# Kernel optimization log

Hardware: AMD Instinct MI355X
Metric: run time of the kernel (lower is better)

Reference implementation:

```python
import jax, jax.numpy as jnp
import numpy as np

B, S, D, H = 2, 4096, 1024, 16
DH = D // H            # head dim = 64
W = 256                # one-sided attention window (attention_window // 2)
NC = S // W            # number of query chunks
NEG = -1e9


def setup_inputs() -> dict:
    key = jax.random.key(0)
    ks = jax.random.split(key, 8)
    sc = 0.02
    return {
        "hidden_states": jax.random.normal(ks[0], (B, S, D), jnp.float32),
        # additive float mask: 0 = local token, <0 = padding, >0 = global. All zeros here.
        "attention_mask": jnp.zeros((B, 1, 1, S), jnp.float32),
        "Wq": jax.random.normal(ks[1], (D, D), jnp.float32) * sc,
        "bq": jnp.zeros((D,), jnp.float32),
        "Wk": jax.random.normal(ks[2], (D, D), jnp.float32) * sc,
        "bk": jnp.zeros((D,), jnp.float32),
        "Wv": jax.random.normal(ks[3], (D, D), jnp.float32) * sc,
        "bv": jnp.zeros((D,), jnp.float32),
        "Wo": jax.random.normal(ks[4], (D, D), jnp.float32) * sc,
        "bo": jnp.zeros((D,), jnp.float32),
    }


def _heads(x, w, b):
    # [B,S,D] -> [B,H,S,DH]
    return (x @ w + b).reshape(B, S, H, DH).transpose(0, 2, 1, 3)


def _forward(hidden_states, attention_mask, Wq, bq, Wk, bk, Wv, bv, Wo, bo):
    mask = attention_mask[:, 0, 0, :]                    # [B,S] additive key mask
    q = _heads(hidden_states, Wq, bq) / jnp.sqrt(jnp.float32(DH))
    k = _heads(hidden_states, Wk, bk)
    v = _heads(hidden_states, Wv, bv)

    # Overlapping key/value chunks: chunk c covers padded positions [c*W, c*W+3W),
    # i.e. global keys [c*W - W, c*W + 2W) -- the union of the windows of its W queries.
    idx = jnp.arange(NC)[:, None] * W + jnp.arange(3 * W)[None, :]   # [NC,3W] into padded axis
    k_pad = jnp.pad(k, ((0, 0), (0, 0), (W, W), (0, 0)))
    v_pad = jnp.pad(v, ((0, 0), (0, 0), (W, W), (0, 0)))
    k_ch = k_pad[:, :, idx]                               # [B,H,NC,3W,DH]
    v_ch = v_pad[:, :, idx]                               # [B,H,NC,3W,DH]
    mask_ch = jnp.pad(mask, ((0, 0), (W, W)))[:, idx]     # [B,NC,3W]

    q_ch = q.reshape(B, H, NC, W, DH)
    scores = jnp.einsum('bhcqd,bhckd->bhcqk', q_ch, k_ch)  # [B,H,NC,W,3W]

    # Band mask: query local p attends key local o with 0 <= o - p <= 2W.
    rel = jnp.arange(3 * W)[None, :] - jnp.arange(W)[:, None]        # [W,3W]
    band = (rel >= 0) & (rel <= 2 * W)
    key_gidx = idx - W                                               # global key index
    valid = (key_gidx >= 0) & (key_gidx < S)                         # [NC,3W]
    allowed = band[None, :, :] & valid[:, None, :]                   # [NC,W,3W]

    scores = scores + mask_ch[:, None, :, None, :]
    scores = jnp.where(allowed[None, None], scores, NEG)
    probs = jax.nn.softmax(scores, axis=-1)

    out = jnp.einsum('bhcqk,bhckd->bhcqd', probs, v_ch)    # [B,H,NC,W,DH]
    out = out.reshape(B, H, S, DH).transpose(0, 2, 1, 3).reshape(B, S, D)
    return out @ Wo + bo


def reference(hidden_states, attention_mask, Wq, bq, Wk, bk, Wv, bv, Wo, bo):
    return _forward(hidden_states, attention_mask, Wq, bq, Wk, bk, Wv, bv, Wo, bo)
```

## Files before the change

kernel.cpp:

```cpp
#include <hip/hip_runtime.h>

typedef unsigned short u16;
typedef __bf16 bf16x8 __attribute__((ext_vector_type(8)));
typedef u16 u16x8 __attribute__((ext_vector_type(8)));
typedef float f32x4 __attribute__((ext_vector_type(4)));

#define LOG2E 1.4426950408889634f

static __device__ __forceinline__ u16 f2bf(float f) {
    union { float f; unsigned u; } x; x.f = f;
    unsigned r = x.u + 0x7fffu + ((x.u >> 16) & 1u);
    return (u16)(r >> 16);
}

static __device__ __forceinline__ void gl_lds16(const void* g, void* l) {
    __builtin_amdgcn_global_load_lds(
        (const __attribute__((address_space(1))) void*)g,
        (__attribute__((address_space(3))) void*)l, 16, 0, 0);
}

__global__ __launch_bounds__(256) void cvt_k(const float* __restrict__ src,
                                             u16* __restrict__ dst, int n) {
    int i = (blockIdx.x * 256 + threadIdx.x) * 4;
    if (i < n) {
        float4 v = *(const float4*)(src + i);
        ushort4 o;
        o.x = f2bf(v.x); o.y = f2bf(v.y); o.z = f2bf(v.z); o.w = f2bf(v.w);
        *(ushort4*)(dst + i) = o;
    }
}

__global__ __launch_bounds__(256) void transw_k(const float* __restrict__ w0,
                                                const float* __restrict__ w1,
                                                const float* __restrict__ w2,
                                                const float* __restrict__ w3,
                                                u16* __restrict__ wt) {
    __shared__ float T[64][65];
    const float* src = (blockIdx.z == 0) ? w0 : (blockIdx.z == 1) ? w1
                     : (blockIdx.z == 2) ? w2 : w3;
    u16* dst = wt + (size_t)blockIdx.z * 1048576;
    const int k0 = blockIdx.x * 64, n0 = blockIdx.y * 64;
    const int rr = threadIdx.x >> 6, col = threadIdx.x & 63;
#pragma unroll
    for (int i = 0; i < 16; ++i) {
        int row = i * 4 + rr;
        T[row][col] = src[(size_t)(k0 + row) * 1024 + n0 + col];
    }
    __syncthreads();
#pragma unroll
    for (int i = 0; i < 16; ++i) {
        int row = i * 4 + rr;
        dst[(size_t)(n0 + row) * 1024 + k0 + col] = f2bf(T[col][row]);
    }
}

__global__ __launch_bounds__(256, 2) void gemm_k(
    const u16* __restrict__ A, const u16* __restrict__ WT0,
    const float* __restrict__ b0, const float* __restrict__ b1,
    const float* __restrict__ b2,
    u16* __restrict__ o0, u16* __restrict__ o1, u16* __restrict__ o2,
    float* __restrict__ oF, int mode) {
    __shared__ alignas(16) u16 Al[128 * 32];
    __shared__ alignas(16) u16 Bl[128 * 32];

    const int tid = threadIdx.x;
    const int lane = tid & 63;
    const int wv = tid >> 6;
    const int wr = wv >> 1, wc = wv & 1;
    const int l15 = lane & 15, l4 = lane >> 4;

    const int mbase = blockIdx.x * 128;
    const int sel = blockIdx.y >> 3;
    const int nb = (blockIdx.y & 7) * 128;

    const u16* Ab = A + (size_t)mbase * 1024;
    const u16* Bb = WT0 + (size_t)sel * 1048576 + (size_t)nb * 1024;

    const int srow = tid >> 2;
    const int scol = (tid & 3) * 8;

    f32x4 acc[4][4] = {};

    for (int k0 = 0; k0 < 1024; k0 += 32) {
        char* la = (char*)Al + wv * 1024;
        char* lb = (char*)Bl + wv * 1024;
        gl_lds16(Ab + (size_t)srow * 1024 + k0 + scol, la);
        gl_lds16(Ab + (size_t)(srow + 64) * 1024 + k0 + scol, la + 4096);
        gl_lds16(Bb + (size_t)srow * 1024 + k0 + scol, lb);
        gl_lds16(Bb + (size_t)(srow + 64) * 1024 + k0 + scol, lb + 4096);
        __syncthreads();

        bf16x8 af[4], bfr[4];
#pragma unroll
        for (int mr = 0; mr < 4; ++mr)
            af[mr] = *(const bf16x8*)(Al + (wr * 64 + mr * 16 + l15) * 32 + l4 * 8);
#pragma unroll
        for (int nr = 0; nr < 4; ++nr)
            bfr[nr] = *(const bf16x8*)(Bl + (wc * 64 + nr * 16 + l15) * 32 + l4 * 8);
#pragma unroll
        for (int mr = 0; mr < 4; ++mr)
#pragma unroll
            for (int nr = 0; nr < 4; ++nr)
                acc[mr][nr] = __builtin_amdgcn_mfma_f32_16x16x32_bf16(
                    af[mr], bfr[nr], acc[mr][nr], 0, 0, 0);
        __syncthreads();
    }

    const float* bias = (sel == 0) ? b0 : ((sel == 1) ? b1 : b2);
    u16* oH = (sel == 0) ? o0 : ((sel == 1) ? o1 : o2);
    const float scale = (mode == 0 && sel == 0) ? 0.125f * LOG2E : 1.0f;

#pragma unroll
    for (int mr = 0; mr < 4; ++mr)
#pragma unroll
        for (int nr = 0; nr < 4; ++nr) {
            int col = nb + wc * 64 + nr * 16 + l15;
            float bv_ = bias[col];
#pragma unroll
            for (int j = 0; j < 4; ++j) {
                int row = mbase + wr * 64 + mr * 16 + l4 * 4 + j;
                float v = (acc[mr][nr][j] + bv_) * scale;
                if (mode == 0) {
                    int b_ = row >> 12, s_ = row & 4095;
                    int h_ = col >> 6, d_ = col & 63;
                    oH[(((size_t)(b_ * 16 + h_) * 4096) + s_) * 64 + d_] = f2bf(v);
                } else {
                    oF[(size_t)row * 1024 + col] = v;
                }
            }
        }
}

__global__ __launch_bounds__(512, 2) void attn_k(
    const u16* __restrict__ Qh, const u16* __restrict__ Kh,
    const u16* __restrict__ Vh, const float* __restrict__ mask,
    u16* __restrict__ attnb) {
    __shared__ alignas(16) u16 Kt[2][4096];
    __shared__ alignas(16) u16 Vt[2][4096];
    __shared__ alignas(16) u16 Pl[8][16][72];
    __shared__ float maskl[2][64];

    const int tid = threadIdx.x;
    const int lane = tid & 63;
    const int wv = tid >> 6;
    const int blk = blockIdx.x;
    const int c = blk & 15;
    const int h = (blk >> 4) & 15;
    const int b = blk >> 8;

    const size_t bh = (size_t)(b * 16 + h) * 4096;
    const u16* Qb = Qh + bh * 64;
    const u16* Kb = Kh + bh * 64;
    const u16* Vb = Vh + bh * 64;

    const int l15 = lane & 15;
    const int l4 = lane >> 4;
    const int qbase = c * 256 + wv * 32;

    bf16x8 qf[2][2];
#pragma unroll
    for (int mr = 0; mr < 2; ++mr) {
        int qs = qbase + mr * 16 + l15;
#pragma unroll
        for (int kk = 0; kk < 2; ++kk)
            qf[mr][kk] = *(const bf16x8*)(Qb + (size_t)qs * 64 + kk * 32 + l4 * 8);
    }

    f32x4 Ov[2][4] = {};
    float lpart[2][4] = {};
    float m = -3.0e38f;

    const int kkey = tid >> 3;
    const int kpos = tid & 7;
    const int vd0 = (tid & 7) * 8;
    const int vbx = (kkey >> 3) ^ (tid & 7);

    const int tmin = wv >> 1;
    const int tmax_t = (wv * 32 + 543) >> 6;

    {
        const int gk0 = c * 256 - 256;
        int gkk = min(max(gk0 + kkey, 0), 4095);
        gl_lds16(Kb + (size_t)gkk * 64 + ((kpos ^ (kkey & 7)) * 8), &Kt[0][wv * 512]);
        u16x8 vv = *(const u16x8*)(Vb + (size_t)gkk * 64 + vd0);
#pragma unroll
        for (int e = 0; e < 8; ++e)
            Vt[0][(vd0 + e) * 64 + ((vbx ^ e) * 8) + (kkey & 7)] = vv[e];
        if (tid < 64) {
            int gm = gk0 + tid;
            maskl[0][tid] = (gm >= 0 && gm < 4096) ? mask[b * 4096 + gm] * LOG2E : -3.0e9f;
        }
    }
    __syncthreads();

    for (int t = 0; t < 12; ++t) {
        const int cur = t & 1, nxt = cur ^ 1;
        const int gk0 = c * 256 - 256 + t * 64;
        const bool pre = (t + 1 < 12);

        u16x8 vv = {};
        float mval = 0.f;
        if (pre) {
            const int gk0n = gk0 + 64;
            int gkk = min(max(gk0n + kkey, 0), 4095);
            gl_lds16(Kb + (size_t)gkk * 64 + ((kpos ^ (kkey & 7)) * 8), &Kt[nxt][wv * 512]);
            vv = *(const u16x8*)(Vb + (size_t)gkk * 64 + vd0);
            if (tid < 64) {
                int gm = gk0n + tid;
                mval = (gm >= 0 && gm < 4096) ? mask[b * 4096 + gm] * LOG2E : -3.0e9f;
            }
        }

        if (t >= tmin && t <= tmax_t) {
            f32x4 sc[2][4] = {};
#pragma unroll
            for (int kk = 0; kk < 2; ++kk)
#pragma unroll
                for (int nr = 0; nr < 4; ++nr) {
                    int r = nr * 16 + l15;
                    bf16x8 kf = *(const bf16x8*)(&Kt[cur][r * 64 + (((kk * 4 + l4) ^ (r & 7)) * 8)]);
                    sc[0][nr] = __builtin_amdgcn_mfma_f32_16x16x32_bf16(qf[0][kk], kf, sc[0][nr], 0, 0, 0);
                    sc[1][nr] = __builtin_amdgcn_mfma_f32_16x16x32_bf16(qf[1][kk], kf, sc[1][nr], 0, 0, 0);
                }

            float amv[4]; int relb[4];
#pragma unroll
            for (int nr = 0; nr < 4; ++nr) {
                amv[nr] = maskl[cur][nr * 16 + l15];
                relb[nr] = gk0 + nr * 16 + l15 - qbase + 256;
            }

            float tmx = -3.0e9f;
#pragma unroll
            for (int mr = 0; mr < 2; ++mr)
#pragma unroll
                for (int nr = 0; nr < 4; ++nr)
#pragma unroll
                    for (int j = 0; j < 4; ++j) {
                        float sv = sc[mr][nr][j] + amv[nr];
                        unsigned u = (unsigned)(relb[nr] - (mr * 16 + l4 * 4 + j));
                        sv = (u <= 512u) ? sv : -3.0e9f;
                        sc[mr][nr][j] = sv;
                        tmx = fmaxf(tmx, sv);
                    }
            tmx = fmaxf(tmx, __shfl_xor(tmx, 1));
            tmx = fmaxf(tmx, __shfl_xor(tmx, 2));
            tmx = fmaxf(tmx, __shfl_xor(tmx, 4));
            tmx = fmaxf(tmx, __shfl_xor(tmx, 8));
            tmx = fmaxf(tmx, __shfl_xor(tmx, 16));
            tmx = fmaxf(tmx, __shfl_xor(tmx, 32));

            if (tmx > m) {
                float alpha = exp2f(m - tmx);
                m = tmx;
#pragma unroll
                for (int mr = 0; mr < 2; ++mr) {
#pragma unroll
                    for (int nd = 0; nd < 4; ++nd) Ov[mr][nd] *= alpha;
#pragma unroll
                    for (int j = 0; j < 4; ++j) lpart[mr][j] *= alpha;
                }
            }

#pragma unroll
            for (int mr = 0; mr < 2; ++mr)
#pragma unroll
                for (int j = 0; j < 4; ++j) {
                    float s0 = 0.f;
#pragma unroll
                    for (int nr = 0; nr < 4; ++nr) {
                        float p = exp2f(sc[mr][nr][j] - m);
                        sc[mr][nr][j] = p;
                        s0 += p;
                    }
                    lpart[mr][j] += s0;
                }

#pragma unroll
            for (int mr = 0; mr < 2; ++mr) {
#pragma unroll
                for (int nr = 0; nr < 4; ++nr)
#pragma unroll
                    for (int j = 0; j < 4; ++j)
                        Pl[wv][l4 * 4 + j][nr * 16 + l15] = f2bf(sc[mr][nr][j]);
#pragma unroll
                for (int kk = 0; kk < 2; ++kk) {
                    bf16x8 pf = *(const bf16x8*)(&Pl[wv][l15][kk * 32 + l4 * 8]);
#pragma unroll
                    for (int nd = 0; nd < 4; ++nd) {
                        int r2 = nd * 16 + l15;
                        bf16x8 vf = *(const bf16x8*)(&Vt[cur][r2 * 64 +
                            (((kk * 4 + l4) ^ (r2 & 7) ^ ((r2 >> 3) & 7)) * 8)]);
                        Ov[mr][nd] = __builtin_amdgcn_mfma_f32_16x16x32_bf16(pf, vf, Ov[mr][nd], 0, 0, 0);
                    }
                }
            }
        }

        if (pre) {
#pragma unroll
            for (int e = 0; e < 8; ++e)
                Vt[nxt][(vd0 + e) * 64 + ((vbx ^ e) * 8) + (kkey & 7)] = vv[e];
            if (tid < 64) maskl[nxt][tid] = mval;
        }
        __syncthreads();
    }

#pragma unroll
    for (int mr = 0; mr < 2; ++mr)
#pragma unroll
        for (int j = 0; j < 4; ++j) {
            float lr = lpart[mr][j];
            lr += __shfl_xor(lr, 1);
            lr += __shfl_xor(lr, 2);
            lr += __shfl_xor(lr, 4);
            lr += __shfl_xor(lr, 8);
            float inv = 1.0f / lr;
            int qs = qbase + mr * 16 + l4 * 4 + j;
            size_t rowb = ((size_t)b * 4096 + qs) * 1024;
#pragma unroll
            for (int nd = 0; nd < 4; ++nd)
                attnb[rowb + h * 64 + nd * 16 + l15] = f2bf(Ov[mr][nd][j] * inv);
        }
}

extern "C" void kernel_launch(void* const* d_in, const int* in_sizes, int n_in,
                              void* d_out, int out_size, void* d_ws, size_t ws_size,
                              hipStream_t stream) {
    (void)in_sizes; (void)n_in; (void)out_size; (void)ws_size;
    const float* hid  = (const float*)d_in[0];
    const float* mask = (const float*)d_in[1];
    const float* Wq = (const float*)d_in[2];
    const float* bq = (const float*)d_in[3];
    const float* Wk = (const float*)d_in[4];
    const float* bk = (const float*)d_in[5];
    const float* Wv = (const float*)d_in[6];
    const float* bv = (const float*)d_in[7];
    const float* Wo = (const float*)d_in[8];
    const float* bo = (const float*)d_in[9];
    float* out = (float*)d_out;

    char* ws = (char*)d_ws;
    u16* hidb  = (u16*)(ws);
    u16* wt    = (u16*)(ws + (16u << 20));
    u16* Qh    = (u16*)(ws + (24u << 20));
    u16* Kh    = (u16*)(ws + (40u << 20));
    u16* Vh    = (u16*)(ws + (56u << 20));
    u16* attnb = (u16*)(ws + (72u << 20));

    cvt_k<<<dim3(8192), dim3(256), 0, stream>>>(hid, hidb, 8388608);
    transw_k<<<dim3(16, 16, 4), dim3(256), 0, stream>>>(Wq, Wk, Wv, Wo, wt);
    gemm_k<<<dim3(64, 24), dim3(256), 0, stream>>>(hidb, wt, bq, bk, bv,
                                                   Qh, Kh, Vh, (float*)nullptr, 0);
    attn_k<<<dim3(512), dim3(512), 0, stream>>>(Qh, Kh, Vh, mask, attnb);
    gemm_k<<<dim3(64, 8), dim3(256), 0, stream>>>(attnb, wt + 3 * 1048576, bo, bo, bo,
                                                  (u16*)nullptr, (u16*)nullptr, (u16*)nullptr,
                                                  out, 1);
}
```

Baseline: 188.2 us.

## Split attention into 128-query blocks with transposed MFMA and packed bf16 conversion

The attention kernel now uses 1024 blocks of 256 threads, each covering 128 queries over 10 key tiles instead of 256 queries over 12, with a blockIdx remap that spreads work across XCDs. Scores are computed transposed (K as the A operand), so softmax row sums need fewer shuffles and outputs are written as packed 4-element stores. Mask values are read straight from global memory instead of staged in LDS, v_cvt_pk_bf16_f32 replaces manual rounding, and s_setprio is raised around the MFMA sections. The aim is better occupancy and fewer idle waves. The cost is that overlapping key tiles are loaded redundantly across neighbouring blocks, raising K/V traffic.

Result: slower. 195.4 us (+3.8%).

```diff
diff --git a/kernel.cpp b/kernel.cpp
--- a/kernel.cpp
+++ b/kernel.cpp
@@ -4,6 +4,7 @@
 typedef __bf16 bf16x8 __attribute__((ext_vector_type(8)));
 typedef u16 u16x8 __attribute__((ext_vector_type(8)));
 typedef float f32x4 __attribute__((ext_vector_type(4)));
+typedef unsigned uint2v __attribute__((ext_vector_type(2)));
 
 #define LOG2E 1.4426950408889634f
 
@@ -11,6 +12,12 @@
     union { float f; unsigned u; } x; x.f = f;
     unsigned r = x.u + 0x7fffu + ((x.u >> 16) & 1u);
     return (u16)(r >> 16);
+}
+
+static __device__ __forceinline__ unsigned cvtpk(float lo, float hi) {
+    unsigned r;
+    asm("v_cvt_pk_bf16_f32 %0, %1, %2" : "=v"(r) : "v"(lo), "v"(hi));
+    return r;
 }
 
 static __device__ __forceinline__ void gl_lds16(const void* g, void* l) {
@@ -131,116 +138,132 @@
         }
 }
 
-__global__ __launch_bounds__(512, 2) void attn_k(
+__global__ __launch_bounds__(256, 3) void attn_k(
     const u16* __restrict__ Qh, const u16* __restrict__ Kh,
     const u16* __restrict__ Vh, const float* __restrict__ mask,
     u16* __restrict__ attnb) {
     __shared__ alignas(16) u16 Kt[2][4096];
     __shared__ alignas(16) u16 Vt[2][4096];
-    __shared__ alignas(16) u16 Pl[8][16][72];
-    __shared__ float maskl[2][64];
+    __shared__ alignas(16) u16 Pl[4][1024];
 
     const int tid = threadIdx.x;
     const int lane = tid & 63;
     const int wv = tid >> 6;
-    const int blk = blockIdx.x;
-    const int c = blk & 15;
-    const int h = (blk >> 4) & 15;
-    const int b = blk >> 8;
+    const int hw = blockIdx.x;
+    const int lg = (hw & 7) * 128 + (hw >> 3);
+    const int c = lg & 31;
+    const int h = (lg >> 5) & 15;
+    const int b = lg >> 9;
 
     const size_t bh = (size_t)(b * 16 + h) * 4096;
     const u16* Qb = Qh + bh * 64;
     const u16* Kb = Kh + bh * 64;
     const u16* Vb = Vh + bh * 64;
+    const float* mb = mask + b * 4096;
 
     const int l15 = lane & 15;
     const int l4 = lane >> 4;
-    const int qbase = c * 256 + wv * 32;
+    const int qbase = c * 128 + wv * 32;
+    const int gkbase = c * 128 - 256;
 
     bf16x8 qf[2][2];
 #pragma unroll
-    for (int mr = 0; mr < 2; ++mr) {
-        int qs = qbase + mr * 16 + l15;
-#pragma unroll
-        for (int kk = 0; kk < 2; ++kk)
-            qf[mr][kk] = *(const bf16x8*)(Qb + (size_t)qs * 64 + kk * 32 + l4 * 8);
-    }
-
-    f32x4 Ov[2][4] = {};
-    float lpart[2][4] = {};
+    for (int qt = 0; qt < 2; ++qt)
+#pragma unroll
+        for (int kc = 0; kc < 2; ++kc)
+            qf[qt][kc] = *(const bf16x8*)(Qb + (size_t)(qbase + qt * 16 + l15) * 64 + kc * 32 + l4 * 8);
+
+    f32x4 Ov[4][2] = {};
+    float lsum[2] = {0.f, 0.f};
     float m = -3.0e38f;
 
-    const int kkey = tid >> 3;
-    const int kpos = tid & 7;
+    const int kslot = lane & 7;
+    const int krow8 = lane >> 3;
+    const int vrow = tid >> 3;
     const int vd0 = (tid & 7) * 8;
-    const int vbx = (kkey >> 3) ^ (tid & 7);
 
     const int tmin = wv >> 1;
-    const int tmax_t = (wv * 32 + 543) >> 6;
+    const int tmax_t = 8 + (wv >> 1);
 
     {
-        const int gk0 = c * 256 - 256;
-        int gkk = min(max(gk0 + kkey, 0), 4095);
-        gl_lds16(Kb + (size_t)gkk * 64 + ((kpos ^ (kkey & 7)) * 8), &Kt[0][wv * 512]);
-        u16x8 vv = *(const u16x8*)(Vb + (size_t)gkk * 64 + vd0);
-#pragma unroll
-        for (int e = 0; e < 8; ++e)
-            Vt[0][(vd0 + e) * 64 + ((vbx ^ e) * 8) + (kkey & 7)] = vv[e];
-        if (tid < 64) {
-            int gm = gk0 + tid;
-            maskl[0][tid] = (gm >= 0 && gm < 4096) ? mask[b * 4096 + gm] * LOG2E : -3.0e9f;
+#pragma unroll
+        for (int i = 0; i < 2; ++i) {
+            int row = i * 32 + wv * 8 + krow8;
+            int key = min(max(gkbase + row, 0), 4095);
+            gl_lds16(Kb + (size_t)key * 64 + ((kslot ^ (row & 7)) * 8),
+                     &Kt[0][(i * 32 + wv * 8) * 64]);
+        }
+#pragma unroll
+        for (int i = 0; i < 2; ++i) {
+            int vk = i * 32 + vrow;
+            int key = min(max(gkbase + vk, 0), 4095);
+            u16x8 vv = *(const u16x8*)(Vb + (size_t)key * 64 + vd0);
+            int vbx = (vk >> 3) ^ (tid & 7);
+#pragma unroll
+            for (int e = 0; e < 8; ++e)
+                Vt[0][(vd0 + e) * 64 + ((vbx ^ e) * 8) + (vk & 7)] = vv[e];
         }
     }
     __syncthreads();
 
-    for (int t = 0; t < 12; ++t) {
+    for (int t = 0; t < 10; ++t) {
         const int cur = t & 1, nxt = cur ^ 1;
-        const int gk0 = c * 256 - 256 + t * 64;
-        const bool pre = (t + 1 < 12);
-
-        u16x8 vv = {};
-        float mval = 0.f;
+        const int gk0 = gkbase + t * 64;
+        const bool pre = (t < 9);
+
+        u16x8 vv[2] = {};
         if (pre) {
             const int gk0n = gk0 + 64;
-            int gkk = min(max(gk0n + kkey, 0), 4095);
-            gl_lds16(Kb + (size_t)gkk * 64 + ((kpos ^ (kkey & 7)) * 8), &Kt[nxt][wv * 512]);
-            vv = *(const u16x8*)(Vb + (size_t)gkk * 64 + vd0);
-            if (tid < 64) {
-                int gm = gk0n + tid;
-                mval = (gm >= 0 && gm < 4096) ? mask[b * 4096 + gm] * LOG2E : -3.0e9f;
+#pragma unroll
+            for (int i = 0; i < 2; ++i) {
+                int row = i * 32 + wv * 8 + krow8;
+                int key = min(max(gk0n + row, 0), 4095);
+                gl_lds16(Kb + (size_t)key * 64 + ((kslot ^ (row & 7)) * 8),
+                         &Kt[nxt][(i * 32 + wv * 8) * 64]);
+            }
+#pragma unroll
+            for (int i = 0; i < 2; ++i) {
+                int key = min(max(gk0n + i * 32 + vrow, 0), 4095);
+                vv[i] = *(const u16x8*)(Vb + (size_t)key * 64 + vd0);
             }
         }
 
         if (t >= tmin && t <= tmax_t) {
-            f32x4 sc[2][4] = {};
-#pragma unroll
-            for (int kk = 0; kk < 2; ++kk)
-#pragma unroll
-                for (int nr = 0; nr < 4; ++nr) {
-                    int r = nr * 16 + l15;
-                    bf16x8 kf = *(const bf16x8*)(&Kt[cur][r * 64 + (((kk * 4 + l4) ^ (r & 7)) * 8)]);
-                    sc[0][nr] = __builtin_amdgcn_mfma_f32_16x16x32_bf16(qf[0][kk], kf, sc[0][nr], 0, 0, 0);
-                    sc[1][nr] = __builtin_amdgcn_mfma_f32_16x16x32_bf16(qf[1][kk], kf, sc[1][nr], 0, 0, 0);
-                }
-
-            float amv[4]; int relb[4];
-#pragma unroll
-            for (int nr = 0; nr < 4; ++nr) {
-                amv[nr] = maskl[cur][nr * 16 + l15];
-                relb[nr] = gk0 + nr * 16 + l15 - qbase + 256;
-            }
+            f32x4 mv[4];
+#pragma unroll
+            for (int kb = 0; kb < 4; ++kb) {
+                int idx = min(max(gk0 + kb * 16 + l4 * 4, 0), 4092);
+                mv[kb] = *(const f32x4*)(mb + idx);
+            }
+
+            f32x4 sc[4][2] = {};
+            __builtin_amdgcn_s_setprio(1);
+#pragma unroll
+            for (int kc = 0; kc < 2; ++kc)
+#pragma unroll
+                for (int kb = 0; kb < 4; ++kb) {
+                    int r = kb * 16 + l15;
+                    bf16x8 kf = *(const bf16x8*)(&Kt[cur][r * 64 + (((kc * 4 + l4) ^ (r & 7)) * 8)]);
+                    sc[kb][0] = __builtin_amdgcn_mfma_f32_16x16x32_bf16(kf, qf[0][kc], sc[kb][0], 0, 0, 0);
+                    sc[kb][1] = __builtin_amdgcn_mfma_f32_16x16x32_bf16(kf, qf[1][kc], sc[kb][1], 0, 0, 0);
+                }
+            __builtin_amdgcn_s_setprio(0);
 
             float tmx = -3.0e9f;
-#pragma unroll
-            for (int mr = 0; mr < 2; ++mr)
-#pragma unroll
-                for (int nr = 0; nr < 4; ++nr)
+            const int kb0 = gk0 + l4 * 4;
+            const int ub0 = kb0 - (qbase + l15) + 256;
+#pragma unroll
+            for (int kb = 0; kb < 4; ++kb)
+#pragma unroll
+                for (int qt = 0; qt < 2; ++qt)
 #pragma unroll
                     for (int j = 0; j < 4; ++j) {
-                        float sv = sc[mr][nr][j] + amv[nr];
-                        unsigned u = (unsigned)(relb[nr] - (mr * 16 + l4 * 4 + j));
-                        sv = (u <= 512u) ? sv : -3.0e9f;
-                        sc[mr][nr][j] = sv;
+                        float sv = fmaf(mv[kb][j], LOG2E, sc[kb][qt][j]);
+                        unsigned band = (unsigned)(ub0 + kb * 16 + j - qt * 16);
+                        unsigned keyv = (unsigned)(kb0 + kb * 16 + j);
+                        bool ok = (band <= 512u) && (keyv < 4096u);
+                        sv = ok ? sv : -3.0e9f;
+                        sc[kb][qt][j] = sv;
                         tmx = fmaxf(tmx, sv);
                     }
             tmx = fmaxf(tmx, __shfl_xor(tmx, 1));
@@ -254,74 +277,86 @@
                 float alpha = exp2f(m - tmx);
                 m = tmx;
 #pragma unroll
-                for (int mr = 0; mr < 2; ++mr) {
-#pragma unroll
-                    for (int nd = 0; nd < 4; ++nd) Ov[mr][nd] *= alpha;
-#pragma unroll
-                    for (int j = 0; j < 4; ++j) lpart[mr][j] *= alpha;
-                }
-            }
-
-#pragma unroll
-            for (int mr = 0; mr < 2; ++mr)
-#pragma unroll
-                for (int j = 0; j < 4; ++j) {
+                for (int nd = 0; nd < 4; ++nd)
+#pragma unroll
+                    for (int qt = 0; qt < 2; ++qt) Ov[nd][qt] *= alpha;
+                lsum[0] *= alpha;
+                lsum[1] *= alpha;
+            }
+
+#pragma unroll
+            for (int kb = 0; kb < 4; ++kb)
+#pragma unroll
+                for (int qt = 0; qt < 2; ++qt) {
                     float s0 = 0.f;
 #pragma unroll
-                    for (int nr = 0; nr < 4; ++nr) {
-                        float p = exp2f(sc[mr][nr][j] - m);
-                        sc[mr][nr][j] = p;
+                    for (int j = 0; j < 4; ++j) {
+                        float p = exp2f(sc[kb][qt][j] - m);
+                        sc[kb][qt][j] = p;
                         s0 += p;
                     }
-                    lpart[mr][j] += s0;
-                }
-
-#pragma unroll
-            for (int mr = 0; mr < 2; ++mr) {
-#pragma unroll
-                for (int nr = 0; nr < 4; ++nr)
-#pragma unroll
-                    for (int j = 0; j < 4; ++j)
-                        Pl[wv][l4 * 4 + j][nr * 16 + l15] = f2bf(sc[mr][nr][j]);
-#pragma unroll
-                for (int kk = 0; kk < 2; ++kk) {
-                    bf16x8 pf = *(const bf16x8*)(&Pl[wv][l15][kk * 32 + l4 * 8]);
+                    lsum[qt] += s0;
+                }
+
+            u16* Pw = &Pl[wv][0];
+            const int prow = l15 * 64;
+#pragma unroll
+            for (int qt = 0; qt < 2; ++qt) {
+#pragma unroll
+                for (int kb = 0; kb < 4; ++kb) {
+                    uint2v pk;
+                    pk[0] = cvtpk(sc[kb][qt][0], sc[kb][qt][1]);
+                    pk[1] = cvtpk(sc[kb][qt][2], sc[kb][qt][3]);
+                    int g = (((kb * 2 + (l4 >> 1)) ^ (l15 & 7)) * 8) + (l4 & 1) * 4;
+                    *(uint2v*)(Pw + prow + g) = pk;
+                }
+#pragma unroll
+                for (int kc = 0; kc < 2; ++kc) {
+                    bf16x8 pf = *(const bf16x8*)(Pw + prow + (((kc * 4 + l4) ^ (l15 & 7)) * 8));
+                    __builtin_amdgcn_s_setprio(1);
 #pragma unroll
                     for (int nd = 0; nd < 4; ++nd) {
                         int r2 = nd * 16 + l15;
                         bf16x8 vf = *(const bf16x8*)(&Vt[cur][r2 * 64 +
-                            (((kk * 4 + l4) ^ (r2 & 7) ^ ((r2 >> 3) & 7)) * 8)]);
-                        Ov[mr][nd] = __builtin_amdgcn_mfma_f32_16x16x32_bf16(pf, vf, Ov[mr][nd], 0, 0, 0);
+                            (((kc * 4 + l4) ^ (r2 & 7) ^ ((r2 >> 3) & 7)) * 8)]);
+                        Ov[nd][qt] = __builtin_amdgcn_mfma_f32_16x16x32_bf16(vf, pf, Ov[nd][qt], 0, 0, 0);
                     }
+                    __builtin_amdgcn_s_setprio(0);
                 }
             }
         }
 
         if (pre) {
 #pragma unroll
-            for (int e = 0; e < 8; ++e)
-                Vt[nxt][(vd0 + e) * 64 + ((vbx ^ e) * 8) + (kkey & 7)] = vv[e];
-            if (tid < 64) maskl[nxt][tid] = mval;
+            for (int i = 0; i < 2; ++i) {
+                int vk = i * 32 + vrow;
+                int vbx = (vk >> 3) ^ (tid & 7);
+#pragma unroll
+                for (int e = 0; e < 8; ++e)
+                    Vt[nxt][(vd0 + e) * 64 + ((vbx ^ e) * 8) + (vk & 7)] = vv[i][e];
+            }
         }
         __syncthreads();
     }
 
-#pragma unroll
-    for (int mr = 0; mr < 2; ++mr)
-#pragma unroll
-        for (int j = 0; j < 4; ++j) {
-            float lr = lpart[mr][j];
-            lr += __shfl_xor(lr, 1);
-            lr += __shfl_xor(lr, 2);
-            lr += __shfl_xor(lr, 4);
-            lr += __shfl_xor(lr, 8);
-            float inv = 1.0f / lr;
-            int qs = qbase + mr * 16 + l4 * 4 + j;
-            size_t rowb = ((size_t)b * 4096 + qs) * 1024;
-#pragma unroll
-            for (int nd = 0; nd < 4; ++nd)
-                attnb[rowb + h * 64 + nd * 16 + l15] = f2bf(Ov[mr][nd][j] * inv);
-        }
+    lsum[0] += __shfl_xor(lsum[0], 16);
+    lsum[0] += __shfl_xor(lsum[0], 32);
+    lsum[1] += __shfl_xor(lsum[1], 16);
+    lsum[1] += __shfl_xor(lsum[1], 32);
+    float inv0 = 1.0f / lsum[0];
+    float inv1 = 1.0f / lsum[1];
+#pragma unroll
+    for (int qt = 0; qt < 2; ++qt) {
+        float inv = qt ? inv1 : inv0;
+        size_t rowb = ((size_t)b * 4096 + qbase + qt * 16 + l15) * 1024 + h * 64 + l4 * 4;
+#pragma unroll
+        for (int nd = 0; nd < 4; ++nd) {
+            uint2v o;
+            o[0] = cvtpk(Ov[nd][qt][0] * inv, Ov[nd][qt][1] * inv);
+            o[1] = cvtpk(Ov[nd][qt][2] * inv, Ov[nd][qt][3] * inv);
+            *(uint2v*)(&attnb[rowb + nd * 16]) = o;
+        }
+    }
 }
 
 extern "C" void kernel_launch(void* const* d_in, const int* in_sizes, int n_in,
@@ -352,7 +387,7 @@
     transw_k<<<dim3(16, 16, 4), dim3(256), 0, stream>>>(Wq, Wk, Wv, Wo, wt);
     gemm_k<<<dim3(64, 24), dim3(256), 0, stream>>>(hidb, wt, bq, bk, bv,
                                                    Qh, Kh, Vh, (float*)nullptr, 0);
-    attn_k<<<dim3(512), dim3(512), 0, stream>>>(Qh, Kh, Vh, mask, attnb);
+    attn_k<<<dim3(1024), dim3(256), 0, stream>>>(Qh, Kh, Vh, mask, attnb);
     gemm_k<<<dim3(64, 8), dim3(256), 0, stream>>>(attnb, wt + 3 * 1048576, bo, bo, bo,
                                                   (u16*)nullptr, (u16*)nullptr, (u16*)nullptr,
                                                   out, 1);
```
